# Kernel optimization log

Measured on AMD Instinct MI355X. Metric: run time of the kernel, lower is better.

The kernel has to match this reference:

```python
import jax, jax.numpy as jnp
import numpy as np

EPS = 1e-8
N_IN, N = 1024, 2048


def _signs():
    # torch picks c1, c2 uniformly from {-1, +1} each call; we use a fixed key
    # so the reference is deterministic.
    r = jax.random.randint(jax.random.key(1234), (2,), 0, 2)
    return (2.0 * r.astype(jnp.float32) - 1.0)


def setup_inputs() -> dict:
    key = jax.random.key(0)
    ks = jax.random.split(key, 6)
    x = jax.random.normal(ks[0], (N_IN,), jnp.float32)
    h_prev = jnp.zeros((N,), jnp.float32)  # module buffer starts at zeros
    W_in = jax.random.uniform(ks[1], (N_IN, N), jnp.float32, -0.1, 0.1)
    W_h = jax.random.uniform(ks[2], (N, N), jnp.float32, -0.1, 0.1)
    bias = jax.random.uniform(ks[3], (N,), jnp.float32, -0.1, 0.1)
    u_prev = jax.random.normal(ks[4], (N_IN + N + 1,), jnp.float32)
    A_prev = jax.random.normal(ks[5], (N, N), jnp.float32)
    return {"x": x, "h_prev": h_prev, "W_in": W_in, "W_h": W_h,
            "bias": bias, "u_prev": u_prev, "A_prev": A_prev}


def reference(x, h_prev, W_in, W_h, bias, u_prev, A_prev):
    n = W_h.shape[0]
    z = x @ W_in + h_prev @ W_h + bias          # [n]
    h_next = jnp.tanh(z)
    dh_dz = 1.0 - h_next * h_next               # [n]
    # diag(dh_dz) @ W_h rewritten as a row-wise broadcast scale (same math)
    H = dh_dz[:, None] * W_h                    # [n, n]
    H_q = H @ A_prev                            # [n, n]
    h_q = jnp.concatenate([x, h_prev, jnp.ones((1,), x.dtype)])  # [n_in+n+1]
    c1, c2 = _signs()
    # ||D||_F == ||dh_dz||_2 since D is diagonal
    p1 = jnp.sqrt(jnp.linalg.norm(H_q) / (EPS + jnp.linalg.norm(u_prev)))
    p2 = jnp.sqrt(jnp.linalg.norm(dh_dz) / (EPS + jnp.linalg.norm(h_q)))
    u_next = c1 * p1 * u_prev + c2 * p2 * h_q
    idx = jnp.arange(n)
    A_next = (c1 / (p1 + EPS)) * H_q
    A_next = A_next.at[idx, idx].add((c2 / (p2 + EPS)) * dh_dz)
    # torch Function returns only h_next; u_next/A_next are forward-computed
    # state saved for backward -- returned here so the work is observable.
    return h_next, u_next, A_next
```

## Files before the change

### kernel.cpp

```cpp
#include <hip/hip_runtime.h>
#include <hip/hip_bf16.h>
#include <math.h>

#define C1 1.0f
#define C2 1.0f

static constexpr float EPSF = 1e-8f;
static constexpr int NIN = 1024;
static constexpr int NH  = 2048;
static constexpr int NU  = NIN + NH + 1;

typedef __attribute__((ext_vector_type(8))) short bf16x8;
typedef __attribute__((ext_vector_type(4))) float f32x4;


__device__ inline unsigned short f2bf(float f) {
  union { float f; unsigned u; } v; v.f = f;
  unsigned r = v.u + 0x7FFFu + ((v.u >> 16) & 1u);
  return (unsigned short)(r >> 16);
}

__device__ inline float blockReduce256(float v, float* red) {
  int t = threadIdx.x;
  red[t] = v;
  __syncthreads();
  for (int s = 128; s > 0; s >>= 1) {
    if (t < s) red[t] += red[t + s];
    __syncthreads();
  }
  float r = red[0];
  __syncthreads();
  return r;
}

__global__ void k_stage1(const float* __restrict__ x, const float* __restrict__ hprev,
                         const float* __restrict__ Win, const float* __restrict__ Wh,
                         float* __restrict__ part,
                         const float* __restrict__ Ap, unsigned short* __restrict__ Bt,
                         const float* __restrict__ u, float* __restrict__ nrm) {
  __shared__ float ls[64][65];
  int b = blockIdx.x;
  int t = threadIdx.x;
  if (b < 256) {
    int bj = b & 7, bi = b >> 3;
    int j = bj * 256 + t;
    int i0 = bi * 96, i1 = i0 + 96;
    float s = 0.f;
    for (int i = i0; i < i1; ++i) {
      if (i < NIN) s += x[i] * Win[(size_t)i * NH + j];
      else         s += hprev[i - NIN] * Wh[(size_t)(i - NIN) * NH + j];
    }
    part[bi * NH + j] = s;
  } else if (b < 1280) {
    int bb = b - 256;
    int tn = bb & 31, tk = bb >> 5;
    int r = t >> 4, c = (t & 15) * 4;
#pragma unroll
    for (int i = 0; i < 4; ++i) {
      float4 v = *(const float4*)&Ap[(size_t)(tk * 64 + r + i * 16) * NH + tn * 64 + c];
      ls[r + i * 16][c] = v.x; ls[r + i * 16][c + 1] = v.y;
      ls[r + i * 16][c + 2] = v.z; ls[r + i * 16][c + 3] = v.w;
    }
    __syncthreads();
#pragma unroll
    for (int i = 0; i < 4; ++i) {
      int n = r + i * 16;
      ushort4 o;
      o.x = f2bf(ls[c][n]);     o.y = f2bf(ls[c + 1][n]);
      o.z = f2bf(ls[c + 2][n]); o.w = f2bf(ls[c + 3][n]);
      *(ushort4*)&Bt[(size_t)(tn * 64 + n) * NH + tk * 64 + c] = o;
    }
  } else {
    float* red = (float*)ls;
    float su = 0, sx = 0, sh = 0;
    for (int i = t; i < NU;  i += 256) su += u[i] * u[i];
    for (int i = t; i < NIN; i += 256) sx += x[i] * x[i];
    for (int i = t; i < NH;  i += 256) sh += hprev[i] * hprev[i];
    float r0 = blockReduce256(su, red);
    float r1 = blockReduce256(sx, red);
    float r2 = blockReduce256(sh, red);
    if (t == 0) { nrm[0] = r0; nrm[1] = r1; nrm[2] = r2; }
  }
}

__global__ void k_z2(const float* __restrict__ part, const float* __restrict__ bias,
                     float* __restrict__ outh, float* __restrict__ dh,
                     float* __restrict__ dhp) {
  __shared__ float red[256];
  int j = blockIdx.x * 256 + threadIdx.x;
  float z = bias[j];
  for (int bi = 0; bi < 32; ++bi) z += part[bi * NH + j];
  float h = tanhf(z);
  outh[j] = h;
  float d = 1.f - h * h;
  dh[j] = d;
  float s = blockReduce256(d * d, red);
  if (threadIdx.x == 0) dhp[blockIdx.x] = s;
}

__global__ void k_prep_a(const float* __restrict__ Wh, const float* __restrict__ dh,
                         unsigned short* __restrict__ Abf) {
  int idx4 = blockIdx.x * 256 + threadIdx.x;
  float4 w = ((const float4*)Wh)[idx4];
  float d = dh[idx4 >> 9];
  ushort4 o;
  o.x = f2bf(w.x * d); o.y = f2bf(w.y * d);
  o.z = f2bf(w.z * d); o.w = f2bf(w.w * d);
  ((ushort4*)Abf)[idx4] = o;
}

#define GLOAD_LDS(gsrc, ldst) \
  __builtin_amdgcn_global_load_lds( \
      (const __attribute__((address_space(1))) unsigned int*)(gsrc), \
      (__attribute__((address_space(3))) unsigned int*)(ldst), 16, 0, 0)

__global__ __launch_bounds__(256) void k_gemm(const unsigned short* __restrict__ Abf,
                                              const unsigned short* __restrict__ Bt,
                                              float* __restrict__ Hq,
                                              float* __restrict__ gp) {
  __shared__ unsigned short As[64 * 32];
  __shared__ unsigned short Bs[64 * 32];
  __shared__ float red[256];
  const int K = NH;
  int t = threadIdx.x;
  int lane = t & 63;
  int bm = blockIdx.x >> 5, bn = blockIdx.x & 31;
  int wid = t >> 6;
  int wr = wid >> 1, wc = wid & 1;

  const unsigned short* Ag = Abf + (size_t)(bm * 64 + (t >> 2)) * K + (t & 3) * 8;
  const unsigned short* Bg = Bt  + (size_t)(bn * 64 + (t >> 2)) * K + (t & 3) * 8;
  unsigned short* AsT = As + t * 8;
  unsigned short* BsT = Bs + t * 8;

  f32x4 acc[2][2] = {};

  for (int k0 = 0; k0 < K; k0 += 32) {
    GLOAD_LDS(Ag + k0, AsT);
    GLOAD_LDS(Bg + k0, BsT);
    __syncthreads();
    bf16x8 af[2], bfr[2];
#pragma unroll
    for (int mi = 0; mi < 2; ++mi)
      af[mi] = *(const bf16x8*)&As[(wr * 32 + mi * 16 + (lane & 15)) * 32 + (lane >> 4) * 8];
#pragma unroll
    for (int ni = 0; ni < 2; ++ni)
      bfr[ni] = *(const bf16x8*)&Bs[(wc * 32 + ni * 16 + (lane & 15)) * 32 + (lane >> 4) * 8];
#pragma unroll
    for (int mi = 0; mi < 2; ++mi)
#pragma unroll
      for (int ni = 0; ni < 2; ++ni)
        acc[mi][ni] = __builtin_amdgcn_mfma_f32_16x16x32_bf16(af[mi], bfr[ni], acc[mi][ni], 0, 0, 0);
    __syncthreads();
  }

  float ss = 0.f;
  int r0 = bm * 64 + wr * 32 + (lane >> 4) * 4;
  int c0 = bn * 64 + wc * 32 + (lane & 15);
#pragma unroll
  for (int mi = 0; mi < 2; ++mi)
#pragma unroll
    for (int r = 0; r < 4; ++r) {
      int row = r0 + mi * 16 + r;
#pragma unroll
      for (int ni = 0; ni < 2; ++ni) {
        float v = acc[mi][ni][r];
        Hq[(size_t)row * NH + c0 + ni * 16] = v;
        ss += v * v;
      }
    }
  float s = blockReduce256(ss, red);
  if (t == 0) gp[blockIdx.x] = s;
}

__global__ void k_Au(float* __restrict__ Hq, const float* __restrict__ dh,
                     const float* __restrict__ gp, const float* __restrict__ dhp,
                     const float* __restrict__ nrm,
                     const float* __restrict__ u, const float* __restrict__ x,
                     const float* __restrict__ hprev, float* __restrict__ outu) {
  __shared__ float red[256];
  __shared__ float cf[4];
  int t = threadIdx.x;
  float s = blockReduce256(gp[t] + gp[t + 256] + gp[t + 512] + gp[t + 768], red);
  if (t == 0) {
    float sdh = 0;
    for (int i = 0; i < 8; ++i) sdh += dhp[i];
    float nu  = sqrtf(nrm[0]);
    float nhq = sqrtf(nrm[1] + nrm[2] + 1.0f);
    float ndh = sqrtf(sdh);
    float nHq = sqrtf(s);
    float p1 = sqrtf(nHq / (EPSF + nu));
    float p2 = sqrtf(ndh / (EPSF + nhq));
    cf[0] = C1 * p1;
    cf[1] = C2 * p2;
    cf[2] = C1 / (p1 + EPSF);
    cf[3] = C2 / (p2 + EPSF);
  }
  __syncthreads();

  if (blockIdx.x >= 2048) {
    int i = (blockIdx.x - 2048) * 256 + t;
    if (i < NU) {
      float hq = (i < NIN) ? x[i] : (i < NIN + NH ? hprev[i - NIN] : 1.0f);
      outu[i] = cf[0] * u[i] + cf[1] * hq;
    }
    return;
  }
  float sA = cf[2], sD = cf[3];
  size_t i = (size_t)blockIdx.x * 256 + t;
  const size_t stride = (size_t)2048 * 256;
#pragma unroll
  for (int it = 0; it < 8; ++it, i += stride) {
    float v = sA * Hq[i];
    int row = (int)(i >> 11), col = (int)(i & 2047);
    if (row == col) v += sD * dh[row];
    Hq[i] = v;
  }
}

extern "C" void kernel_launch(void* const* d_in, const int* in_sizes, int n_in,
                              void* d_out, int out_size, void* d_ws, size_t ws_size,
                              hipStream_t stream) {
  const float* x     = (const float*)d_in[0];
  const float* hprev = (const float*)d_in[1];
  const float* Win   = (const float*)d_in[2];
  const float* Wh    = (const float*)d_in[3];
  const float* bias  = (const float*)d_in[4];
  const float* uprev = (const float*)d_in[5];
  const float* Ap    = (const float*)d_in[6];

  float* out  = (float*)d_out;
  float* outh = out;
  float* outu = out + NH;
  float* Hq   = out + NH + NU;
  float* part = Hq;

  char* ws = (char*)d_ws;
  float* dh   = (float*)ws;
  float* dhp  = (float*)(ws + 8192);
  float* gp   = (float*)(ws + 8256);
  float* nrm  = (float*)(ws + 12352);
  unsigned short* Abf = (unsigned short*)(ws + 16384);
  unsigned short* Bt  = (unsigned short*)(ws + 8404992);

  k_stage1 <<<1281, 256, 0, stream>>>(x, hprev, Win, Wh, part, Ap, Bt, uprev, nrm);
  k_z2     <<<8,    256, 0, stream>>>(part, bias, outh, dh, dhp);
  k_prep_a <<<4096, 256, 0, stream>>>(Wh, dh, Abf);
  k_gemm   <<<1024, 256, 0, stream>>>(Abf, Bt, Hq, gp);
  k_Au     <<<2061, 256, 0, stream>>>(Hq, dh, gp, dhp, nrm, uprev, x, hprev, outu);
}
```

Before: 72.67 us.

## Fuse z-reduction into Wh scaling kernel and deepen GEMM k-tile with swizzled LDS

Merges the small tanh/dh kernel into the bf16 prep kernel, so each prep block recomputes its row's dh from the partial sums instead of waiting on a separate 8-block launch. The GEMM now loads a 64-wide k-slice per iteration into an XOR-swizzled LDS layout, which halves barrier count and is meant to avoid bank conflicts. It also raises wave priority around the MFMA section. The cost is redundant recomputation of z for every row (two blocks per row) and larger shared-memory tiles.

```diff
diff --git a/kernel.cpp b/kernel.cpp
--- a/kernel.cpp
+++ b/kernel.cpp
@@ -83,30 +83,43 @@
   }
 }
 
-__global__ void k_z2(const float* __restrict__ part, const float* __restrict__ bias,
-                     float* __restrict__ outh, float* __restrict__ dh,
-                     float* __restrict__ dhp) {
+__global__ void k_prep(const float* __restrict__ Wh, const float* __restrict__ part,
+                       const float* __restrict__ bias,
+                       unsigned short* __restrict__ Abf,
+                       float* __restrict__ outh, float* __restrict__ dh,
+                       float* __restrict__ dhp) {
   __shared__ float red[256];
-  int j = blockIdx.x * 256 + threadIdx.x;
-  float z = bias[j];
-  for (int bi = 0; bi < 32; ++bi) z += part[bi * NH + j];
-  float h = tanhf(z);
-  outh[j] = h;
-  float d = 1.f - h * h;
-  dh[j] = d;
-  float s = blockReduce256(d * d, red);
-  if (threadIdx.x == 0) dhp[blockIdx.x] = s;
-}
-
-__global__ void k_prep_a(const float* __restrict__ Wh, const float* __restrict__ dh,
-                         unsigned short* __restrict__ Abf) {
-  int idx4 = blockIdx.x * 256 + threadIdx.x;
-  float4 w = ((const float4*)Wh)[idx4];
-  float d = dh[idx4 >> 9];
-  ushort4 o;
-  o.x = f2bf(w.x * d); o.y = f2bf(w.y * d);
-  o.z = f2bf(w.z * d); o.w = f2bf(w.w * d);
-  ((ushort4*)Abf)[idx4] = o;
+  __shared__ float dhs;
+  int b = blockIdx.x, t = threadIdx.x;
+  if (b < 4096) {
+    int r = b >> 1;
+    if (t < 32) red[t] = part[t * NH + r];
+    __syncthreads();
+    if (t == 0) {
+      float z = bias[r];
+      for (int i = 0; i < 32; ++i) z += red[i];
+      float h = tanhf(z);
+      dhs = 1.f - h * h;
+    }
+    __syncthreads();
+    float d = dhs;
+    int idx4 = b * 256 + t;
+    float4 w = ((const float4*)Wh)[idx4];
+    ushort4 o;
+    o.x = f2bf(w.x * d); o.y = f2bf(w.y * d);
+    o.z = f2bf(w.z * d); o.w = f2bf(w.w * d);
+    ((ushort4*)Abf)[idx4] = o;
+  } else {
+    int j = (b - 4096) * 256 + t;
+    float z = bias[j];
+    for (int bi = 0; bi < 32; ++bi) z += part[bi * NH + j];
+    float h = tanhf(z);
+    outh[j] = h;
+    float d = 1.f - h * h;
+    dh[j] = d;
+    float s = blockReduce256(d * d, red);
+    if (t == 0) dhp[b - 4096] = s;
+  }
 }
 
 #define GLOAD_LDS(gsrc, ldst) \
@@ -118,8 +131,8 @@
                                               const unsigned short* __restrict__ Bt,
                                               float* __restrict__ Hq,
                                               float* __restrict__ gp) {
-  __shared__ unsigned short As[64 * 32];
-  __shared__ unsigned short Bs[64 * 32];
+  __shared__ unsigned short As[512 * 8];
+  __shared__ unsigned short Bs[512 * 8];
   __shared__ float red[256];
   const int K = NH;
   int t = threadIdx.x;
@@ -128,29 +141,42 @@
   int wid = t >> 6;
   int wr = wid >> 1, wc = wid & 1;
 
-  const unsigned short* Ag = Abf + (size_t)(bm * 64 + (t >> 2)) * K + (t & 3) * 8;
-  const unsigned short* Bg = Bt  + (size_t)(bn * 64 + (t >> 2)) * K + (t & 3) * 8;
-  unsigned short* AsT = As + t * 8;
-  unsigned short* BsT = Bs + t * 8;
+  int srow = t >> 3, skg = t & 7;
+  int sx = skg ^ (srow & 7);
+  const unsigned short* AgBase = Abf + (size_t)(bm * 64 + srow) * K + sx * 8;
+  const unsigned short* BgBase = Bt  + (size_t)(bn * 64 + srow) * K + sx * 8;
 
   f32x4 acc[2][2] = {};
 
-  for (int k0 = 0; k0 < K; k0 += 32) {
-    GLOAD_LDS(Ag + k0, AsT);
-    GLOAD_LDS(Bg + k0, BsT);
-    __syncthreads();
-    bf16x8 af[2], bfr[2];
-#pragma unroll
-    for (int mi = 0; mi < 2; ++mi)
-      af[mi] = *(const bf16x8*)&As[(wr * 32 + mi * 16 + (lane & 15)) * 32 + (lane >> 4) * 8];
-#pragma unroll
-    for (int ni = 0; ni < 2; ++ni)
-      bfr[ni] = *(const bf16x8*)&Bs[(wc * 32 + ni * 16 + (lane & 15)) * 32 + (lane >> 4) * 8];
-#pragma unroll
-    for (int mi = 0; mi < 2; ++mi)
-#pragma unroll
-      for (int ni = 0; ni < 2; ++ni)
-        acc[mi][ni] = __builtin_amdgcn_mfma_f32_16x16x32_bf16(af[mi], bfr[ni], acc[mi][ni], 0, 0, 0);
+  for (int k0 = 0; k0 < K; k0 += 64) {
+    GLOAD_LDS(AgBase + k0,          As + t * 8);
+    GLOAD_LDS(AgBase + 32 * K + k0, As + (t + 256) * 8);
+    GLOAD_LDS(BgBase + k0,          Bs + t * 8);
+    GLOAD_LDS(BgBase + 32 * K + k0, Bs + (t + 256) * 8);
+    __syncthreads();
+    __builtin_amdgcn_s_setprio(1);
+#pragma unroll
+    for (int kk = 0; kk < 2; ++kk) {
+      bf16x8 af[2], bfr[2];
+#pragma unroll
+      for (int mi = 0; mi < 2; ++mi) {
+        int row = wr * 32 + mi * 16 + (lane & 15);
+        int kg = (kk * 4 + (lane >> 4)) ^ (row & 7);
+        af[mi] = *(const bf16x8*)&As[(row * 8 + kg) * 8];
+      }
+#pragma unroll
+      for (int ni = 0; ni < 2; ++ni) {
+        int row = wc * 32 + ni * 16 + (lane & 15);
+        int kg = (kk * 4 + (lane >> 4)) ^ (row & 7);
+        bfr[ni] = *(const bf16x8*)&Bs[(row * 8 + kg) * 8];
+      }
+#pragma unroll
+      for (int mi = 0; mi < 2; ++mi)
+#pragma unroll
+        for (int ni = 0; ni < 2; ++ni)
+          acc[mi][ni] = __builtin_amdgcn_mfma_f32_16x16x32_bf16(af[mi], bfr[ni], acc[mi][ni], 0, 0, 0);
+    }
+    __builtin_amdgcn_s_setprio(0);
     __syncthreads();
   }
 
@@ -244,8 +270,7 @@
   unsigned short* Bt  = (unsigned short*)(ws + 8404992);
 
   k_stage1 <<<1281, 256, 0, stream>>>(x, hprev, Win, Wh, part, Ap, Bt, uprev, nrm);
-  k_z2     <<<8,    256, 0, stream>>>(part, bias, outh, dh, dhp);
-  k_prep_a <<<4096, 256, 0, stream>>>(Wh, dh, Abf);
+  k_prep   <<<4104, 256, 0, stream>>>(Wh, part, bias, Abf, outh, dh, dhp);
   k_gemm   <<<1024, 256, 0, stream>>>(Abf, Bt, Hq, gp);
   k_Au     <<<2061, 256, 0, stream>>>(Hq, dh, gp, dhp, nrm, uprev, x, hprev, outu);
 }
```

Result: faster. 62.30 us (-14.3%).
